# Kernel optimization log

Measured on AMD Instinct MI355X. Metric: run time of the kernel, lower is better.

Reference implementation:

```python
import jax, jax.numpy as jnp
import numpy as np

NUM_HEADS = 16
EPS = 1e-12  # matches torch F.normalize eps


def _l2norm(t):
    n = jnp.sqrt(jnp.sum(t * t, axis=-1, keepdims=True))
    return t / jnp.maximum(n, EPS)


def setup_inputs() -> dict:
    key = jax.random.key(0)
    kx, kq, kk, kv = jax.random.split(key, 4)
    B, S, E = 2, 2048, 1024
    head_dim = E // NUM_HEADS
    bound = 1.0 / np.sqrt(E)  # nn.Linear default init range
    x = jax.random.normal(kx, (B, S, E), dtype=jnp.float32)
    Wq = jax.random.uniform(kq, (E, E), dtype=jnp.float32, minval=-bound, maxval=bound)
    Wk = jax.random.uniform(kk, (E, E), dtype=jnp.float32, minval=-bound, maxval=bound)
    Wv = jax.random.uniform(kv, (E, E), dtype=jnp.float32, minval=-bound, maxval=bound)
    g_scale = jnp.asarray(np.sqrt(head_dim), dtype=jnp.float32)  # 1/d_k = sqrt(head_dim)
    return {"x": x, "Wq": Wq, "Wk": Wk, "Wv": Wv, "g_scale": g_scale}


def reference(x, Wq, Wk, Wv, g_scale):
    B, S, E = x.shape
    H = NUM_HEADS
    D = E // H
    # projections (torch Linear: x @ W.T), split heads -> [B, H, S, D]
    q = (x @ Wq.T).reshape(B, S, H, D).transpose(0, 2, 1, 3)
    k = (x @ Wk.T).reshape(B, S, H, D).transpose(0, 2, 1, 3)
    v = (x @ Wv.T).reshape(B, S, H, D).transpose(0, 2, 1, 3)
    # qk_norm branch: L2-normalize q, k then learnable scale
    q = _l2norm(q)
    k = _l2norm(k)
    scores = g_scale * jnp.einsum('bhqd,bhkd->bhqk', q, k)  # [B, H, S, S]
    attn = jax.nn.softmax(scores, axis=-1)
    # dropout p=0.0 (eval) -> identity
    out = jnp.einsum('bhqk,bhkd->bhqd', attn, v)  # [B, H, S, D]
    out = out.transpose(0, 2, 1, 3).reshape(B, S, E)
    return out
```

## Files before the change

### kernel.cpp

```cpp
#include <hip/hip_runtime.h>
#include <math.h>

#define NH 16
#define HD 64
#define SEQ 2048
#define BAT 2
#define EMB 1024
#define MTOT (BAT*SEQ)
#define NTOT (3*EMB)

typedef __attribute__((ext_vector_type(8))) short bf16x8;
typedef __attribute__((ext_vector_type(4))) float f32x4;

#define MFMA16(a,b,c) __builtin_amdgcn_mfma_f32_16x16x32_bf16(a,b,c,0,0,0)

__device__ inline short f2bf(float f) {
    union { float f; unsigned u; } x; x.f = f;
    unsigned r = (x.u + 0x7FFF + ((x.u >> 16) & 1)) >> 16;
    return (short)r;
}

__device__ inline float fast_exp2(float x) {
#if __has_builtin(__builtin_amdgcn_exp2f)
    return __builtin_amdgcn_exp2f(x);
#else
    float r; asm("v_exp_f32 %0, %1" : "=v"(r) : "v"(x)); return r;
#endif
}

__device__ inline unsigned pack2bf(float a, float b) {
    union { float f; unsigned u; } x, y; x.f = a; y.f = b;
    return __builtin_amdgcn_perm(y.u + 0x8000u, x.u + 0x8000u, 0x07060302u);
}

typedef const __attribute__((address_space(1))) void* gp_t;
typedef __attribute__((address_space(3))) void* lp_t;
__device__ inline void gload16(const void* g, void* l) {
    __builtin_amdgcn_global_load_lds((gp_t)(uintptr_t)g, (lp_t)(uintptr_t)l, 16, 0, 0);
}

__global__ __launch_bounds__(256) void prep_kernel(
    const float* __restrict__ x, const float* __restrict__ wq,
    const float* __restrict__ wk, const float* __restrict__ wv,
    short* __restrict__ xb, short* __restrict__ wb)
{
    const size_t NX = (size_t)MTOT * EMB;
    const size_t NW = (size_t)EMB * EMB;
    const size_t i4 = ((size_t)blockIdx.x * 256 + threadIdx.x) * 4;
    float4 v; short* dst;
    if (i4 < NX) { v = *(const float4*)(x + i4); dst = xb + i4; }
    else {
        size_t j = i4 - NX;
        const float* s = (j < NW) ? wq : (j < 2 * NW) ? wk : wv;
        v = *(const float4*)(s + (j & (NW - 1)));
        dst = wb + j;
    }
    short4 o; o.x = f2bf(v.x); o.y = f2bf(v.y); o.z = f2bf(v.z); o.w = f2bf(v.w);
    *(short4*)dst = o;
}

__global__ __launch_bounds__(256) void qkv_gemm_fast(
    const short* __restrict__ xb, const short* __restrict__ wb,
    short* __restrict__ qws, short* __restrict__ kws, short* __restrict__ vperm,
    const float* __restrict__ gptr)
{
    __shared__ short As[128 * 64];
    __shared__ short Bs[128 * 64];
    const int m0 = blockIdx.x * 128, n0 = blockIdx.y * 128;
    const int t = threadIdx.x, wave = t >> 6, lane = t & 63;
    const int quad = lane >> 4, l16 = lane & 15;
    const int wm = (wave & 1) * 64, wn = (wave >> 1) * 64;

    const int srow = wave * 32 + (lane >> 3);
    const int scol = ((lane & 7) ^ (srow & 7)) * 8;
    const short* ga = xb + (size_t)(m0 + srow) * EMB + scol;
    const short* gb = wb + (size_t)(n0 + srow) * EMB + scol;
    short* lA = As + (size_t)wave * 2048;
    short* lB = Bs + (size_t)wave * 2048;

    const short* Aa[2]; const short* Ba[2];
#pragma unroll
    for (int ks = 0; ks < 2; ++ks) {
        const int pc = (ks * 32 + quad * 8) ^ ((l16 & 7) * 8);
        Aa[ks] = As + (wm + l16) * 64 + pc;
        Ba[ks] = Bs + (wn + l16) * 64 + pc;
    }

    f32x4 acc[4][4] = {};

    for (int k0 = 0; k0 < EMB; k0 += 64) {
#pragma unroll
        for (int j = 0; j < 4; ++j) {
            gload16(ga + k0 + (size_t)j * 8 * EMB, lA + j * 512);
            gload16(gb + k0 + (size_t)j * 8 * EMB, lB + j * 512);
        }
        __syncthreads();
#pragma unroll
        for (int ks = 0; ks < 2; ++ks) {
            bf16x8 af[4], bfr[4];
#pragma unroll
            for (int i = 0; i < 4; ++i) af[i]  = *(const bf16x8*)(Aa[ks] + i * 1024);
#pragma unroll
            for (int i = 0; i < 4; ++i) bfr[i] = *(const bf16x8*)(Ba[ks] + i * 1024);
#pragma unroll
            for (int mf = 0; mf < 4; ++mf)
#pragma unroll
                for (int nf = 0; nf < 4; ++nf)
                    acc[mf][nf] = MFMA16(af[mf], bfr[nf], acc[mf][nf]);
        }
        __syncthreads();
    }

    const int mat = n0 >> 10;
    if (mat < 2) {
        const float scale = (mat == 0) ? gptr[0] * 1.4426950408889634f : 1.0f;
        float inv[4][4];
#pragma unroll
        for (int mf = 0; mf < 4; ++mf)
#pragma unroll
            for (int reg = 0; reg < 4; ++reg) {
                float ss = 0.f;
#pragma unroll
                for (int nf = 0; nf < 4; ++nf) { float v = acc[mf][nf][reg]; ss += v * v; }
                ss += __shfl_xor(ss, 1, 16);
                ss += __shfl_xor(ss, 2, 16);
                ss += __shfl_xor(ss, 4, 16);
                ss += __shfl_xor(ss, 8, 16);
                inv[mf][reg] = scale / fmaxf(sqrtf(ss), 1e-12f);
            }
        short* outp = (mat == 0) ? qws : kws;
#pragma unroll
        for (int mf = 0; mf < 4; ++mf)
#pragma unroll
            for (int nf = 0; nf < 4; ++nf) {
                const int cw = (n0 & 1023) + wn + nf * 16 + l16;
                const int h = cw >> 6, d = cw & 63;
#pragma unroll
                for (int reg = 0; reg < 4; ++reg) {
                    const int s = m0 + wm + mf * 16 + quad * 4 + reg;
                    const int b = s >> 11, sl = s & (SEQ - 1);
                    outp[(((size_t)(b * NH + h) * SEQ + sl) * HD) + d] =
                        f2bf(acc[mf][nf][reg] * inv[mf][reg]);
                }
            }
    } else {
#pragma unroll
        for (int mf = 0; mf < 4; ++mf)
#pragma unroll
            for (int nf = 0; nf < 4; ++nf) {
                const int cw = (n0 & 1023) + wn + nf * 16 + l16;
                const int h = cw >> 6, d = cw & 63;
                const int s = m0 + wm + mf * 16 + quad * 4;
                const int b = s >> 11, sl = s & (SEQ - 1);
                const int pos = (sl & ~31) + ((sl & 12) >> 2) * 8 + ((sl >> 4) & 1) * 4;
                short4 o;
                o.x = f2bf(acc[mf][nf][0]); o.y = f2bf(acc[mf][nf][1]);
                o.z = f2bf(acc[mf][nf][2]); o.w = f2bf(acc[mf][nf][3]);
                *(short4*)&vperm[(((size_t)(b * NH + h) * HD + d) * SEQ) + pos] = o;
            }
    }
}

__global__ __launch_bounds__(256) void attn_kernel(
    const short* __restrict__ qws, const short* __restrict__ kws,
    const short* __restrict__ vperm, float* __restrict__ out)
{
    __shared__ short Kt[2][128 * 64];
    __shared__ short Vt[2][64 * 128];
    const int id = blockIdx.x;
    const int bh = id & 31, qt = id >> 5;
    const int b = bh >> 4, h = bh & (NH - 1);
    const size_t base = (size_t)bh * SEQ * HD;
    const int t = threadIdx.x, wave = t >> 6, lane = t & 63;
    const int quad = lane >> 4, l16 = lane & 15;

    bf16x8 bq[2][2];
    {
        const short* qp = qws + base + (size_t)(qt * 128 + wave * 32 + l16) * HD + quad * 8;
        bq[0][0] = *(const bf16x8*)(qp);
        bq[0][1] = *(const bf16x8*)(qp + 32);
        bq[1][0] = *(const bf16x8*)(qp + 16 * HD);
        bq[1][1] = *(const bf16x8*)(qp + 16 * HD + 32);
    }
    bf16x8 ones;
#pragma unroll
    for (int i = 0; i < 8; ++i) ones[i] = (short)0x3F80;

    const int krow = wave * 32 + (lane >> 3);
    const int kcol = ((lane & 7) ^ (krow & 7)) * 8;
    const int vd = wave * 16 + (lane >> 4);
    const int vg = (lane & 15);

    int pcK[2], pcV[4];
#pragma unroll
    for (int ks = 0; ks < 2; ++ks)
        pcK[ks] = l16 * 64 + ((ks * 32 + quad * 8) ^ ((l16 & 7) * 8));
#pragma unroll
    for (int g = 0; g < 4; ++g)
        pcV[g] = l16 * 128 + (((g * 4 + quad) ^ l16) * 8);

    f32x4 o_acc[2][4] = {};
    f32x4 l_acc[2] = {};

    auto stage = [&](int kt, int p) {
        const short* kg = kws + base + (size_t)(kt * 128 + krow) * HD + kcol;
        short* lK = &Kt[p][0] + (size_t)wave * 2048;
        short* lV = &Vt[p][0] + (size_t)wave * 2048;
#pragma unroll
        for (int j = 0; j < 4; ++j)
            gload16(kg + (size_t)j * 8 * HD, lK + j * 512);
#pragma unroll
        for (int j = 0; j < 4; ++j) {
            const int d = vd + j * 4;
            const int lg = vg ^ (d & 15);
            gload16(vperm + base + (size_t)d * SEQ + kt * 128 + lg * 8, lV + j * 512);
        }
    };

    stage(0, 0);
    __syncthreads();

    for (int kt = 0; kt < SEQ / 128; ++kt) {
        const int p = kt & 1;
        if (kt + 1 < SEQ / 128) stage(kt + 1, p ^ 1);
        const short* Kp = &Kt[p][0];
        const short* Vp = &Vt[p][0];

#pragma unroll
        for (int g = 0; g < 4; ++g) {
            f32x4 st[2][2];
#pragma unroll
            for (int pp = 0; pp < 2; ++pp) {
                const int tau = 2 * g + pp;
                bf16x8 a0 = *(const bf16x8*)(Kp + pcK[0] + tau * 1024);
                bf16x8 a1 = *(const bf16x8*)(Kp + pcK[1] + tau * 1024);
#pragma unroll
                for (int qs = 0; qs < 2; ++qs) {
                    f32x4 z = {};
                    z = MFMA16(a0, bq[qs][0], z);
                    st[pp][qs] = MFMA16(a1, bq[qs][1], z);
                }
            }
            bf16x8 vf[4];
#pragma unroll
            for (int nt = 0; nt < 4; ++nt)
                vf[nt] = *(const bf16x8*)(Vp + pcV[g] + nt * 2048);
#pragma unroll
            for (int qs = 0; qs < 2; ++qs) {
                bf16x8 pa;
                unsigned* pu = (unsigned*)&pa;
                pu[0] = pack2bf(fast_exp2(st[0][qs][0]), fast_exp2(st[0][qs][1]));
                pu[1] = pack2bf(fast_exp2(st[0][qs][2]), fast_exp2(st[0][qs][3]));
                pu[2] = pack2bf(fast_exp2(st[1][qs][0]), fast_exp2(st[1][qs][1]));
                pu[3] = pack2bf(fast_exp2(st[1][qs][2]), fast_exp2(st[1][qs][3]));
                l_acc[qs] = MFMA16(pa, ones, l_acc[qs]);
#pragma unroll
                for (int nt = 0; nt < 4; ++nt)
                    o_acc[qs][nt] = MFMA16(pa, vf[nt], o_acc[qs][nt]);
            }
        }
        __syncthreads();
    }

    float linv[2][4];
#pragma unroll
    for (int qs = 0; qs < 2; ++qs)
#pragma unroll
        for (int r = 0; r < 4; ++r)
            linv[qs][r] = 1.0f / l_acc[qs][r];

    float* ob = out + ((size_t)b * SEQ + qt * 128 + wave * 32 + quad * 4) * EMB + h * HD + l16;
#pragma unroll
    for (int qs = 0; qs < 2; ++qs)
#pragma unroll
        for (int nt = 0; nt < 4; ++nt)
#pragma unroll
            for (int r = 0; r < 4; ++r)
                ob[(size_t)(qs * 16 + r) * EMB + nt * 16] = o_acc[qs][nt][r] * linv[qs][r];
}

extern "C" void kernel_launch(void* const* d_in, const int* in_sizes, int n_in,
                              void* d_out, int out_size, void* d_ws, size_t ws_size,
                              hipStream_t stream) {
    (void)in_sizes; (void)n_in; (void)out_size; (void)ws_size;
    const float* x  = (const float*)d_in[0];
    const float* Wq = (const float*)d_in[1];
    const float* Wk = (const float*)d_in[2];
    const float* Wv = (const float*)d_in[3];
    const float* g  = (const float*)d_in[4];
    float* out = (float*)d_out;

    const size_t per = (size_t)BAT * NH * SEQ * HD;
    short* qws   = (short*)d_ws;
    short* kws   = qws + per;
    short* vperm = kws + per;

    short* xb = (short*)out;
    short* wb = xb + (size_t)MTOT * EMB;

    prep_kernel<<<7168, 256, 0, stream>>>(x, Wq, Wk, Wv, xb, wb);
    qkv_gemm_fast<<<dim3(MTOT / 128, NTOT / 128), 256, 0, stream>>>(
        xb, wb, qws, kws, vperm, g);
    attn_kernel<<<(SEQ / 128) * BAT * NH, 256, 0, stream>>>(qws, kws, vperm, out);
}
```

Baseline: 163.5 us.

## Split attention keys across wave pairs and halve query tile per block

The attention kernel now processes 64 queries per block instead of 128, doubling the grid to 1024 blocks. Within a block, waves are paired so each pair covers 32 queries and each wave in the pair handles one half of every 64-key tile. Partial output and row-sum accumulators are combined through shared memory at the end. The aim is better occupancy and load balance on the many CUs, with launch bounds requesting 3 blocks per SM. In exchange, K/V tiles are loaded from global memory twice as often per query and the kernel gains a final reduction step.

```diff
diff --git a/kernel.cpp b/kernel.cpp
--- a/kernel.cpp
+++ b/kernel.cpp
@@ -161,122 +161,147 @@
     }
 }
 
-__global__ __launch_bounds__(256) void attn_kernel(
+__global__ __launch_bounds__(256, 3) void attn_kernel(
     const short* __restrict__ qws, const short* __restrict__ kws,
     const short* __restrict__ vperm, float* __restrict__ out)
 {
-    __shared__ short Kt[2][128 * 64];
-    __shared__ short Vt[2][64 * 128];
+    __shared__ short Kt[2][2][2048];
+    __shared__ short Vt[2][2][2048];
+    __shared__ float lbuf[64];
+
     const int id = blockIdx.x;
     const int bh = id & 31, qt = id >> 5;
     const int b = bh >> 4, h = bh & (NH - 1);
     const size_t base = (size_t)bh * SEQ * HD;
     const int t = threadIdx.x, wave = t >> 6, lane = t & 63;
     const int quad = lane >> 4, l16 = lane & 15;
+    const int qh = wave >> 1, kh = wave & 1;
 
     bf16x8 bq[2][2];
-    {
-        const short* qp = qws + base + (size_t)(qt * 128 + wave * 32 + l16) * HD + quad * 8;
-        bq[0][0] = *(const bf16x8*)(qp);
-        bq[0][1] = *(const bf16x8*)(qp + 32);
-        bq[1][0] = *(const bf16x8*)(qp + 16 * HD);
-        bq[1][1] = *(const bf16x8*)(qp + 16 * HD + 32);
+#pragma unroll
+    for (int qsub = 0; qsub < 2; ++qsub) {
+        const short* qp = qws + base +
+            (size_t)(qt * 64 + qh * 32 + qsub * 16 + l16) * HD + quad * 8;
+        bq[qsub][0] = *(const bf16x8*)(qp);
+        bq[qsub][1] = *(const bf16x8*)(qp + 32);
     }
     bf16x8 ones;
 #pragma unroll
     for (int i = 0; i < 8; ++i) ones[i] = (short)0x3F80;
 
-    const int krow = wave * 32 + (lane >> 3);
-    const int kcol = ((lane & 7) ^ (krow & 7)) * 8;
-    const int vd = wave * 16 + (lane >> 4);
-    const int vg = (lane & 15);
-
-    int pcK[2], pcV[4];
-#pragma unroll
-    for (int ks = 0; ks < 2; ++ks)
-        pcK[ks] = l16 * 64 + ((ks * 32 + quad * 8) ^ ((l16 & 7) * 8));
-#pragma unroll
-    for (int g = 0; g < 4; ++g)
-        pcV[g] = l16 * 128 + (((g * 4 + quad) ^ l16) * 8);
+    int koff[2][2];
+#pragma unroll
+    for (int msub = 0; msub < 2; ++msub)
+#pragma unroll
+        for (int ks = 0; ks < 2; ++ks)
+            koff[msub][ks] = (msub * 16 + l16) * 64 + (((ks * 4 + quad) ^ (l16 & 7)) * 8);
+    int voff[4];
+#pragma unroll
+    for (int nt = 0; nt < 4; ++nt) {
+        const int d = nt * 16 + l16;
+        voff[nt] = d * 32 + ((quad ^ ((d >> 1) & 3)) * 8);
+    }
 
     f32x4 o_acc[2][4] = {};
     f32x4 l_acc[2] = {};
 
-    auto stage = [&](int kt, int p) {
-        const short* kg = kws + base + (size_t)(kt * 128 + krow) * HD + kcol;
-        short* lK = &Kt[p][0] + (size_t)wave * 2048;
-        short* lV = &Vt[p][0] + (size_t)wave * 2048;
-#pragma unroll
-        for (int j = 0; j < 4; ++j)
-            gload16(kg + (size_t)j * 8 * HD, lK + j * 512);
-#pragma unroll
-        for (int j = 0; j < 4; ++j) {
-            const int d = vd + j * 4;
-            const int lg = vg ^ (d & 15);
-            gload16(vperm + base + (size_t)d * SEQ + kt * 128 + lg * 8, lV + j * 512);
+    auto stage = [&](int tt, int p) {
+        if (qh == 0) {
+#pragma unroll
+            for (int j = 0; j < 4; ++j) {
+                const int kl = j * 8 + (lane >> 3);
+                const int row = tt * 64 + kh * 32 + kl;
+                gload16(kws + base + (size_t)row * HD + (((lane & 7) ^ (kl & 7)) * 8),
+                        &Kt[p][kh][j * 512 + lane * 8]);
+            }
+        } else {
+#pragma unroll
+            for (int j = 0; j < 4; ++j) {
+                const int d = j * 16 + (lane >> 2);
+                const int ug = (lane & 3) ^ ((d >> 1) & 3);
+                gload16(vperm + base + (size_t)d * SEQ + tt * 64 + kh * 32 + ug * 8,
+                        &Vt[p][kh][j * 512 + lane * 8]);
+            }
         }
     };
 
     stage(0, 0);
     __syncthreads();
 
-    for (int kt = 0; kt < SEQ / 128; ++kt) {
-        const int p = kt & 1;
-        if (kt + 1 < SEQ / 128) stage(kt + 1, p ^ 1);
-        const short* Kp = &Kt[p][0];
-        const short* Vp = &Vt[p][0];
-
-#pragma unroll
-        for (int g = 0; g < 4; ++g) {
-            f32x4 st[2][2];
-#pragma unroll
-            for (int pp = 0; pp < 2; ++pp) {
-                const int tau = 2 * g + pp;
-                bf16x8 a0 = *(const bf16x8*)(Kp + pcK[0] + tau * 1024);
-                bf16x8 a1 = *(const bf16x8*)(Kp + pcK[1] + tau * 1024);
-#pragma unroll
-                for (int qs = 0; qs < 2; ++qs) {
-                    f32x4 z = {};
-                    z = MFMA16(a0, bq[qs][0], z);
-                    st[pp][qs] = MFMA16(a1, bq[qs][1], z);
+    for (int tt = 0; tt < SEQ / 64; ++tt) {
+        const int p = tt & 1;
+        if (tt + 1 < SEQ / 64) stage(tt + 1, p ^ 1);
+        const short* Kp = &Kt[p][kh][0];
+        const short* Vp = &Vt[p][kh][0];
+
+        f32x4 st[2][2];
+#pragma unroll
+        for (int msub = 0; msub < 2; ++msub) {
+            bf16x8 a0 = *(const bf16x8*)(Kp + koff[msub][0]);
+            bf16x8 a1 = *(const bf16x8*)(Kp + koff[msub][1]);
+#pragma unroll
+            for (int qsub = 0; qsub < 2; ++qsub) {
+                f32x4 z = {};
+                z = MFMA16(a0, bq[qsub][0], z);
+                st[msub][qsub] = MFMA16(a1, bq[qsub][1], z);
+            }
+        }
+        bf16x8 vf[4];
+#pragma unroll
+        for (int nt = 0; nt < 4; ++nt)
+            vf[nt] = *(const bf16x8*)(Vp + voff[nt]);
+#pragma unroll
+        for (int qsub = 0; qsub < 2; ++qsub) {
+            bf16x8 pa;
+            unsigned* pu = (unsigned*)&pa;
+            pu[0] = pack2bf(fast_exp2(st[0][qsub][0]), fast_exp2(st[0][qsub][1]));
+            pu[1] = pack2bf(fast_exp2(st[0][qsub][2]), fast_exp2(st[0][qsub][3]));
+            pu[2] = pack2bf(fast_exp2(st[1][qsub][0]), fast_exp2(st[1][qsub][1]));
+            pu[3] = pack2bf(fast_exp2(st[1][qsub][2]), fast_exp2(st[1][qsub][3]));
+            l_acc[qsub] = MFMA16(pa, ones, l_acc[qsub]);
+#pragma unroll
+            for (int nt = 0; nt < 4; ++nt)
+                o_acc[qsub][nt] = MFMA16(pa, vf[nt], o_acc[qsub][nt]);
+        }
+        __syncthreads();
+    }
+
+    float* red = (float*)&Kt[0][0][0];
+    if (kh == 1) {
+#pragma unroll
+        for (int qsub = 0; qsub < 2; ++qsub) {
+#pragma unroll
+            for (int nt = 0; nt < 4; ++nt)
+#pragma unroll
+                for (int r = 0; r < 4; ++r)
+                    red[qh * 2048 + (qsub * 16 + quad * 4 + r) * 64 + nt * 16 + l16] =
+                        o_acc[qsub][nt][r];
+            if (l16 == 0)
+#pragma unroll
+                for (int r = 0; r < 4; ++r)
+                    lbuf[qh * 32 + qsub * 16 + quad * 4 + r] = l_acc[qsub][r];
+        }
+    }
+    __syncthreads();
+    if (kh == 0) {
+#pragma unroll
+        for (int qsub = 0; qsub < 2; ++qsub) {
+            float linv[4];
+#pragma unroll
+            for (int r = 0; r < 4; ++r)
+                linv[r] = 1.0f / (l_acc[qsub][r] + lbuf[qh * 32 + qsub * 16 + quad * 4 + r]);
+            const int s = qt * 64 + qh * 32 + qsub * 16 + quad * 4;
+            float* ob = out + ((size_t)b * SEQ + s) * EMB + h * HD + l16;
+#pragma unroll
+            for (int nt = 0; nt < 4; ++nt)
+#pragma unroll
+                for (int r = 0; r < 4; ++r) {
+                    const float o = o_acc[qsub][nt][r] +
+                        red[qh * 2048 + (qsub * 16 + quad * 4 + r) * 64 + nt * 16 + l16];
+                    ob[(size_t)r * EMB + nt * 16] = o * linv[r];
                 }
-            }
-            bf16x8 vf[4];
-#pragma unroll
-            for (int nt = 0; nt < 4; ++nt)
-                vf[nt] = *(const bf16x8*)(Vp + pcV[g] + nt * 2048);
-#pragma unroll
-            for (int qs = 0; qs < 2; ++qs) {
-                bf16x8 pa;
-                unsigned* pu = (unsigned*)&pa;
-                pu[0] = pack2bf(fast_exp2(st[0][qs][0]), fast_exp2(st[0][qs][1]));
-                pu[1] = pack2bf(fast_exp2(st[0][qs][2]), fast_exp2(st[0][qs][3]));
-                pu[2] = pack2bf(fast_exp2(st[1][qs][0]), fast_exp2(st[1][qs][1]));
-                pu[3] = pack2bf(fast_exp2(st[1][qs][2]), fast_exp2(st[1][qs][3]));
-                l_acc[qs] = MFMA16(pa, ones, l_acc[qs]);
-#pragma unroll
-                for (int nt = 0; nt < 4; ++nt)
-                    o_acc[qs][nt] = MFMA16(pa, vf[nt], o_acc[qs][nt]);
-            }
-        }
-        __syncthreads();
-    }
-
-    float linv[2][4];
-#pragma unroll
-    for (int qs = 0; qs < 2; ++qs)
-#pragma unroll
-        for (int r = 0; r < 4; ++r)
-            linv[qs][r] = 1.0f / l_acc[qs][r];
-
-    float* ob = out + ((size_t)b * SEQ + qt * 128 + wave * 32 + quad * 4) * EMB + h * HD + l16;
-#pragma unroll
-    for (int qs = 0; qs < 2; ++qs)
-#pragma unroll
-        for (int nt = 0; nt < 4; ++nt)
-#pragma unroll
-            for (int r = 0; r < 4; ++r)
-                ob[(size_t)(qs * 16 + r) * EMB + nt * 16] = o_acc[qs][nt][r] * linv[qs][r];
+        }
+    }
 }
 
 extern "C" void kernel_launch(void* const* d_in, const int* in_sizes, int n_in,
@@ -301,5 +326,5 @@
     prep_kernel<<<7168, 256, 0, stream>>>(x, Wq, Wk, Wv, xb, wb);
     qkv_gemm_fast<<<dim3(MTOT / 128, NTOT / 128), 256, 0, stream>>>(
         xb, wb, qws, kws, vperm, g);
-    attn_kernel<<<(SEQ / 128) * BAT * NH, 256, 0, stream>>>(qws, kws, vperm, out);
-}
+    attn_kernel<<<(SEQ / 64) * BAT * NH, 256, 0, stream>>>(qws, kws, vperm, out);
+}
```

Measured after the change: 164.2 us. About the same (+0.4%).
